# Optimization experiments

Hardware: AMD Instinct MI355X
Metric: run time of the kernel (lower is better)

The kernel has to match this reference:

```python
import jax, jax.numpy as jnp
import numpy as np

N_NODES = 20000
N_EDGES = 320000
IN_DIM = 512
NUM_CLASSES = 10
DROP_P = 0.2


def _gcn_conv(x, src, dst, W, b, n):
    # PyG GCNConv: linear transform, add self-loops, symmetric deg^-1/2 norm,
    # scatter-add into destination nodes, then bias.
    h = x @ W                                   # [N, out]
    loops = jnp.arange(n)
    s = jnp.concatenate([src, loops])           # source (j)
    d = jnp.concatenate([dst, loops])           # destination (i)
    deg = jax.ops.segment_sum(jnp.ones_like(s, dtype=h.dtype), d, num_segments=n)
    dinv = jax.lax.rsqrt(deg)                   # deg >= 1 thanks to self-loops
    norm = dinv[s] * dinv[d]                    # [E+N]
    msg = h[s] * norm[:, None]                  # gather + per-edge scale
    out = jax.ops.segment_sum(msg, d, num_segments=n)  # scatter-add
    return out + b


def _dropout(x, key, p=DROP_P):
    keep = jax.random.bernoulli(key, 1.0 - p, x.shape)
    return jnp.where(keep, x / (1.0 - p), jnp.zeros((), x.dtype))


def setup_inputs() -> dict:
    key = jax.random.key(0)
    ks = jax.random.split(key, 6)
    x = jax.random.normal(ks[0], (N_NODES, IN_DIM), dtype=jnp.float32)
    edge_index = jax.random.randint(ks[1], (2, N_EDGES), 0, N_NODES, dtype=jnp.int64)
    h1, h2 = IN_DIM // 2, IN_DIM // 4
    W1 = jax.random.normal(ks[2], (IN_DIM, h1), dtype=jnp.float32) / np.sqrt(IN_DIM)
    W2 = jax.random.normal(ks[3], (h1, h2), dtype=jnp.float32) / np.sqrt(h1)
    W3 = jax.random.normal(ks[4], (h2, NUM_CLASSES), dtype=jnp.float32) / np.sqrt(h2)
    b1 = jnp.zeros((h1,), jnp.float32)
    b2 = jnp.zeros((h2,), jnp.float32)
    b3 = jnp.zeros((NUM_CLASSES,), jnp.float32)
    return {"x": x, "edge_index": edge_index, "W1": W1, "b1": b1,
            "W2": W2, "b2": b2, "W3": W3, "b3": b3}


def reference(x, edge_index, W1, b1, W2, b2, W3, b3):
    n = x.shape[0]
    src, dst = edge_index[0], edge_index[1]
    dk1, dk2 = jax.random.split(jax.random.key(1))
    h = _gcn_conv(x, src, dst, W1, b1, n)
    h = _dropout(jax.nn.relu(h), dk1)
    h = _gcn_conv(h, src, dst, W2, b2, n)
    h = _dropout(jax.nn.relu(h), dk2)
    h = _gcn_conv(h, src, dst, W3, b3, n)
    return jax.nn.log_softmax(h, axis=1)
```

## Files before the change

### kernel.cpp

```cpp
#include <hip/hip_runtime.h>
#include <hip/hip_bf16.h>
#include <math.h>

typedef __attribute__((ext_vector_type(8))) short short8;
typedef __attribute__((ext_vector_type(8))) unsigned short ushort8;
typedef __attribute__((ext_vector_type(4))) unsigned short ushort4v;
typedef __attribute__((ext_vector_type(2))) unsigned short ushort2v;
typedef __attribute__((ext_vector_type(4))) float f32x4;

__host__ __device__ inline void threefry2x32(unsigned k0, unsigned k1,
                                             unsigned x0, unsigned x1,
                                             unsigned* out0, unsigned* out1) {
  unsigned ks0 = k0, ks1 = k1, ks2 = k0 ^ k1 ^ 0x1BD11BDAu;
  x0 += ks0; x1 += ks1;
#define TF_ROUND(r) { x0 += x1; x1 = (x1 << (r)) | (x1 >> (32 - (r))); x1 ^= x0; }
  TF_ROUND(13) TF_ROUND(15) TF_ROUND(26) TF_ROUND(6)
  x0 += ks1; x1 += ks2 + 1u;
  TF_ROUND(17) TF_ROUND(29) TF_ROUND(16) TF_ROUND(24)
  x0 += ks2; x1 += ks0 + 2u;
  TF_ROUND(13) TF_ROUND(15) TF_ROUND(26) TF_ROUND(6)
  x0 += ks0; x1 += ks1 + 3u;
  TF_ROUND(17) TF_ROUND(29) TF_ROUND(16) TF_ROUND(24)
  x0 += ks1; x1 += ks2 + 4u;
  TF_ROUND(13) TF_ROUND(15) TF_ROUND(26) TF_ROUND(6)
  x0 += ks2; x1 += ks0 + 5u;
#undef TF_ROUND
  *out0 = x0; *out1 = x1;
}

__device__ inline float jax_uniform01(unsigned key0, unsigned key1, unsigned i) {
  unsigned o0, o1;
  threefry2x32(key0, key1, 0u, i, &o0, &o1);
  unsigned bits = o0 ^ o1;
  return __uint_as_float((bits >> 9) | 0x3f800000u) - 1.0f;
}

__device__ inline unsigned short f2bf(float f) {
  unsigned u = __float_as_uint(f);
  u += 0x7fffu + ((u >> 16) & 1u);
  return (unsigned short)(u >> 16);
}

__device__ inline float bf2f(unsigned short b) {
  return __uint_as_float(((unsigned)b) << 16);
}

__global__ void k_zero(int* p, int n) {
  int i = blockIdx.x * blockDim.x + threadIdx.x;
  if (i < n) p[i] = 0;
}

__global__ void k_deg(const int* __restrict__ ei, int E, int* __restrict__ deg) {
  int e = blockIdx.x * blockDim.x + threadIdx.x;
  if (e >= E) return;
  atomicAdd(&deg[ei[E + e]], 1);
}

__global__ void k_scan(const int* __restrict__ deg, int* __restrict__ off, int n) {
  __shared__ int sums[1024];
  int t = threadIdx.x;
  int per = (n + 1023) >> 10;
  int base = t * per;
  int s = 0;
  for (int j = 0; j < per; ++j) { int idx = base + j; if (idx < n) s += deg[idx]; }
  sums[t] = s;
  __syncthreads();
  for (int d = 1; d < 1024; d <<= 1) {
    int v = (t >= d) ? sums[t - d] : 0;
    __syncthreads();
    sums[t] += v;
    __syncthreads();
  }
  int prefix = (t == 0) ? 0 : sums[t - 1];
  for (int j = 0; j < per; ++j) {
    int idx = base + j;
    if (idx < n) { off[idx] = prefix; prefix += deg[idx]; }
  }
  if (t == 1023) off[n] = sums[1023];
}

__global__ void k_prep(const int* __restrict__ deg, const int* __restrict__ off,
                       int* __restrict__ cur, float* __restrict__ dinv, int n) {
  int i = blockIdx.x * blockDim.x + threadIdx.x;
  if (i >= n) return;
  cur[i] = off[i];
  dinv[i] = 1.0f / sqrtf((float)(deg[i] + 1));
}

__global__ void k_fill(const int* __restrict__ ei, int E,
                       int* __restrict__ cur, int* __restrict__ srcs) {
  int e = blockIdx.x * blockDim.x + threadIdx.x;
  if (e >= E) return;
  int s = ei[e];
  int d = ei[E + e];
  int pos = atomicAdd(&cur[d], 1);
  srcs[pos] = s;
}

__global__ void k_cvt_wT(const float* __restrict__ W, unsigned short* __restrict__ WT,
                         int K, int N) {
  int idx = blockIdx.x * blockDim.x + threadIdx.x;
  if (idx >= K * N) return;
  int k = idx / N, n = idx % N;
  WT[(size_t)n * K + k] = f2bf(W[idx]);
}

template <bool AF32, bool OBF>
__global__ __launch_bounds__(256) void k_gemm_mfma(const void* __restrict__ Ap,
                                                   const unsigned short* __restrict__ BT,
                                                   void* __restrict__ Cp,
                                                   int M, int N, int K) {
  __shared__ unsigned short As[64][40];
  __shared__ unsigned short Bs[128][40];
  const int tid = threadIdx.x;
  const int row0 = blockIdx.y * 64;
  const int col0 = blockIdx.x * 128;
  const int w = tid >> 6, lane = tid & 63;
  const int wm = w >> 1, wn = w & 1;
  const int lr = lane & 15, lk = lane >> 4;

  f32x4 acc[2][4];
#pragma unroll
  for (int mi = 0; mi < 2; ++mi)
#pragma unroll
    for (int ni = 0; ni < 4; ++ni) acc[mi][ni] = (f32x4)0.0f;

  const int ar = tid >> 2;
  const int aseg = (tid & 3) * 8;

  for (int k0 = 0; k0 < K; k0 += 32) {
    {
      int grow = row0 + ar;
      ushort8 av = (ushort8)0;
      if (grow < M) {
        if (AF32) {
          const float* A = (const float*)Ap;
          const float* p = &A[(size_t)grow * K + k0 + aseg];
          float4 v0 = *(const float4*)p;
          float4 v1 = *(const float4*)(p + 4);
          av[0] = f2bf(v0.x); av[1] = f2bf(v0.y); av[2] = f2bf(v0.z); av[3] = f2bf(v0.w);
          av[4] = f2bf(v1.x); av[5] = f2bf(v1.y); av[6] = f2bf(v1.z); av[7] = f2bf(v1.w);
        } else {
          const unsigned short* A = (const unsigned short*)Ap;
          av = *(const ushort8*)&A[(size_t)grow * K + k0 + aseg];
        }
      }
      *(ushort8*)&As[ar][aseg] = av;
    }
#pragma unroll
    for (int p = 0; p < 2; ++p) {
      int u = tid + p * 256;
      int br = u >> 2;
      int bseg = (u & 3) * 8;
      ushort8 bv = *(const ushort8*)&BT[(size_t)(col0 + br) * K + k0 + bseg];
      *(ushort8*)&Bs[br][bseg] = bv;
    }
    __syncthreads();

    short8 a[2], b[4];
#pragma unroll
    for (int mi = 0; mi < 2; ++mi)
      a[mi] = *(const short8*)&As[wm * 32 + mi * 16 + lr][lk * 8];
#pragma unroll
    for (int ni = 0; ni < 4; ++ni)
      b[ni] = *(const short8*)&Bs[wn * 64 + ni * 16 + lr][lk * 8];
#pragma unroll
    for (int mi = 0; mi < 2; ++mi)
#pragma unroll
      for (int ni = 0; ni < 4; ++ni)
        acc[mi][ni] = __builtin_amdgcn_mfma_f32_16x16x32_bf16(a[mi], b[ni], acc[mi][ni], 0, 0, 0);
    __syncthreads();
  }

#pragma unroll
  for (int mi = 0; mi < 2; ++mi) {
    int rbase = row0 + wm * 32 + mi * 16 + lk * 4;
#pragma unroll
    for (int j = 0; j < 4; ++j) {
      int row = rbase + j;
      if (row < M) {
#pragma unroll
        for (int ni = 0; ni < 4; ++ni) {
          int col = col0 + wn * 64 + ni * 16 + lr;
          if (OBF) {
            ((unsigned short*)Cp)[(size_t)row * N + col] = f2bf(acc[mi][ni][j]);
          } else {
            ((float*)Cp)[(size_t)row * N + col] = acc[mi][ni][j];
          }
        }
      }
    }
  }
}

__global__ __launch_bounds__(256) void k_gemm(const float* __restrict__ A,
                                              const float* __restrict__ B,
                                              float* __restrict__ C,
                                              int M, int N, int K) {
  __shared__ float As[64][17];
  __shared__ float Bs[16][64];
  const int tid = threadIdx.x;
  const int tx = tid & 15, ty = tid >> 4;
  const int row0 = blockIdx.y * 64, col0 = blockIdx.x * 64;
  const int am = tid >> 2;
  const int aq = (tid & 3) * 4;
  const int bk = tid >> 4;
  const int bg = (tid & 15) * 4;
  const bool nvec = ((N & 3) == 0);
  float acc[4][4] = {{0.f}};

  for (int k0 = 0; k0 < K; k0 += 16) {
    {
      int row = row0 + am;
      if (row < M) {
        const float4 v = *reinterpret_cast<const float4*>(&A[(size_t)row * K + k0 + aq]);
        As[am][aq + 0] = v.x; As[am][aq + 1] = v.y;
        As[am][aq + 2] = v.z; As[am][aq + 3] = v.w;
      } else {
        As[am][aq + 0] = 0.f; As[am][aq + 1] = 0.f;
        As[am][aq + 2] = 0.f; As[am][aq + 3] = 0.f;
      }
    }
    {
      int krow = k0 + bk;
      if (nvec && (col0 + bg + 4 <= N)) {
        const float4 v = *reinterpret_cast<const float4*>(&B[(size_t)krow * N + col0 + bg]);
        Bs[bk][bg + 0] = v.x; Bs[bk][bg + 1] = v.y;
        Bs[bk][bg + 2] = v.z; Bs[bk][bg + 3] = v.w;
      } else {
        for (int j = 0; j < 4; ++j) {
          int col = col0 + bg + j;
          Bs[bk][bg + j] = (col < N) ? B[(size_t)krow * N + col] : 0.f;
        }
      }
    }
    __syncthreads();
#pragma unroll
    for (int kk = 0; kk < 16; ++kk) {
      float a0 = As[ty * 4 + 0][kk];
      float a1 = As[ty * 4 + 1][kk];
      float a2 = As[ty * 4 + 2][kk];
      float a3 = As[ty * 4 + 3][kk];
      float4 bv = *reinterpret_cast<const float4*>(&Bs[kk][tx * 4]);
      acc[0][0] += a0 * bv.x; acc[0][1] += a0 * bv.y; acc[0][2] += a0 * bv.z; acc[0][3] += a0 * bv.w;
      acc[1][0] += a1 * bv.x; acc[1][1] += a1 * bv.y; acc[1][2] += a1 * bv.z; acc[1][3] += a1 * bv.w;
      acc[2][0] += a2 * bv.x; acc[2][1] += a2 * bv.y; acc[2][2] += a2 * bv.z; acc[2][3] += a2 * bv.w;
      acc[3][0] += a3 * bv.x; acc[3][1] += a3 * bv.y; acc[3][2] += a3 * bv.z; acc[3][3] += a3 * bv.w;
    }
    __syncthreads();
  }

  for (int i = 0; i < 4; ++i) {
    int row = row0 + ty * 4 + i;
    if (row >= M) continue;
    for (int j = 0; j < 4; ++j) {
      int col = col0 + tx * 4 + j;
      if (col < N) C[(size_t)row * N + col] = acc[i][j];
    }
  }
}

template <int C, bool OBF>
__global__ __launch_bounds__(256) void k_agg_bf(const unsigned short* __restrict__ h,
                                                void* __restrict__ outv,
                                                const int* __restrict__ off,
                                                const int* __restrict__ srcs,
                                                const float* __restrict__ dinv,
                                                const float* __restrict__ bias,
                                                unsigned key0, unsigned key1, int n) {
  typedef __attribute__((ext_vector_type(C))) unsigned short ushortC;
  const int node = blockIdx.x * (blockDim.x >> 6) + (threadIdx.x >> 6);
  if (node >= n) return;
  const int lane = threadIdx.x & 63;
  const int F = 64 * C;
  const float dv = dinv[node];

  float acc[C];
  {
    ushortC r = *(const ushortC*)(h + (size_t)node * F + lane * C);
    float wv = dv * dv;
#pragma unroll
    for (int j = 0; j < C; ++j) acc[j] = bf2f(r[j]) * wv;
  }
  int e = off[node];
  const int e1 = off[node + 1];
  for (; e + 4 <= e1; e += 4) {
    int s0 = srcs[e + 0], s1 = srcs[e + 1], s2 = srcs[e + 2], s3 = srcs[e + 3];
    float w0 = dinv[s0] * dv, w1 = dinv[s1] * dv, w2 = dinv[s2] * dv, w3 = dinv[s3] * dv;
    ushortC r0 = *(const ushortC*)(h + (size_t)s0 * F + lane * C);
    ushortC r1 = *(const ushortC*)(h + (size_t)s1 * F + lane * C);
    ushortC r2 = *(const ushortC*)(h + (size_t)s2 * F + lane * C);
    ushortC r3 = *(const ushortC*)(h + (size_t)s3 * F + lane * C);
#pragma unroll
    for (int j = 0; j < C; ++j)
      acc[j] += bf2f(r0[j]) * w0 + bf2f(r1[j]) * w1 + bf2f(r2[j]) * w2 + bf2f(r3[j]) * w3;
  }
  for (; e < e1; ++e) {
    int s = srcs[e];
    float wv = dinv[s] * dv;
    ushortC r = *(const ushortC*)(h + (size_t)s * F + lane * C);
#pragma unroll
    for (int j = 0; j < C; ++j) acc[j] += bf2f(r[j]) * wv;
  }
#pragma unroll
  for (int j = 0; j < C; ++j) {
    float v = acc[j] + bias[lane * C + j];
    v = fmaxf(v, 0.0f);
    unsigned i = (unsigned)(node * F + lane * C + j);
    float u = jax_uniform01(key0, key1, i);
    v = (u < 0.8f) ? (v * 1.25f) : 0.0f;
    acc[j] = v;
  }
  if (OBF) {
    unsigned short* op = (unsigned short*)outv + (size_t)node * F + lane * C;
#pragma unroll
    for (int j = 0; j < C; ++j) op[j] = f2bf(acc[j]);
  } else {
    float* op = (float*)outv + (size_t)node * F + lane * C;
#pragma unroll
    for (int j = 0; j < C; ++j) op[j] = acc[j];
  }
}

__global__ void k_agg3_lsm(const float* __restrict__ h, float* __restrict__ out,
                           const int* __restrict__ off, const int* __restrict__ srcs,
                           const float* __restrict__ dinv, const float* __restrict__ b,
                           int n) {
  int d = blockIdx.x * blockDim.x + threadIdx.x;
  if (d >= n) return;
  float acc[10];
  float dv = dinv[d];
#pragma unroll
  for (int f = 0; f < 10; ++f) acc[f] = h[(size_t)d * 10 + f] * dv * dv;
  int e1 = off[d + 1];
  for (int e = off[d]; e < e1; ++e) {
    int s = srcs[e];
    float w = dinv[s] * dv;
#pragma unroll
    for (int f = 0; f < 10; ++f) acc[f] += h[(size_t)s * 10 + f] * w;
  }
  float m = -1e30f;
#pragma unroll
  for (int f = 0; f < 10; ++f) { acc[f] += b[f]; m = fmaxf(m, acc[f]); }
  float sum = 0.f;
#pragma unroll
  for (int f = 0; f < 10; ++f) sum += expf(acc[f] - m);
  float lse = m + logf(sum);
#pragma unroll
  for (int f = 0; f < 10; ++f) out[(size_t)d * 10 + f] = acc[f] - lse;
}

extern "C" void kernel_launch(void* const* d_in, const int* in_sizes, int n_in,
                              void* d_out, int out_size, void* d_ws, size_t ws_size,
                              hipStream_t stream) {
  const float* x  = (const float*)d_in[0];
  const int*   ei = (const int*)d_in[1];
  const float* W1 = (const float*)d_in[2];
  const float* b1 = (const float*)d_in[3];
  const float* W2 = (const float*)d_in[4];
  const float* b2 = (const float*)d_in[5];
  const float* W3 = (const float*)d_in[6];
  const float* b3 = (const float*)d_in[7];
  float* out = (float*)d_out;

  const int N = 20000;
  const int E = in_sizes[1] / 2;
  const int D1 = 256, D2 = 128;

  char* ws = (char*)d_ws;
  auto carve = [&](size_t bytes) -> char* {
    char* p = ws;
    ws += (bytes + 255) & ~(size_t)255;
    return p;
  };
  int*   deg  = (int*)carve((size_t)N * 4);
  int*   off  = (int*)carve((size_t)(N + 1) * 4);
  int*   cur  = (int*)carve((size_t)N * 4);
  float* dinv = (float*)carve((size_t)N * 4);
  int*   srcs = (int*)carve((size_t)E * 4);
  unsigned short* W1T = (unsigned short*)carve((size_t)D1 * 512 * 2);
  unsigned short* W2T = (unsigned short*)carve((size_t)D2 * D1 * 2);
  unsigned short* bufHb = (unsigned short*)carve((size_t)N * D1 * 2);
  unsigned short* bufA_bf = (unsigned short*)carve((size_t)N * D1 * 2);
  float* bufA2 = (float*)bufA_bf;
  float* bufH3 = (float*)carve((size_t)N * 10 * 4);

  unsigned dk1_0, dk1_1, dk2_0, dk2_1;
  threefry2x32(0u, 1u, 0u, 0u, &dk1_0, &dk1_1);
  threefry2x32(0u, 1u, 0u, 1u, &dk2_0, &dk2_1);

  k_zero<<<(N + 255) / 256, 256, 0, stream>>>(deg, N);
  k_deg<<<(E + 255) / 256, 256, 0, stream>>>(ei, E, deg);
  k_scan<<<1, 1024, 0, stream>>>(deg, off, N);
  k_prep<<<(N + 255) / 256, 256, 0, stream>>>(deg, off, cur, dinv, N);
  k_fill<<<(E + 255) / 256, 256, 0, stream>>>(ei, E, cur, srcs);
  k_cvt_wT<<<(512 * D1 + 255) / 256, 256, 0, stream>>>(W1, W1T, 512, D1);
  k_cvt_wT<<<(D1 * D2 + 255) / 256, 256, 0, stream>>>(W2, W2T, D1, D2);

  k_gemm_mfma<true, true><<<dim3(D1 / 128, (N + 63) / 64), 256, 0, stream>>>(x, W1T, bufHb, N, D1, 512);
  k_agg_bf<4, true><<<(N + 3) / 4, 256, 0, stream>>>(bufHb, bufA_bf, off, srcs, dinv, b1, dk1_0, dk1_1, N);

  k_gemm_mfma<false, true><<<dim3(D2 / 128, (N + 63) / 64), 256, 0, stream>>>(bufA_bf, W2T, bufHb, N, D2, D1);
  k_agg_bf<2, false><<<(N + 3) / 4, 256, 0, stream>>>(bufHb, bufA2, off, srcs, dinv, b2, dk2_0, dk2_1, N);

  k_gemm<<<dim3(1, (N + 63) / 64), 256, 0, stream>>>(bufA2, W3, bufH3, N, 10, D2);
  k_agg3_lsm<<<(N + 127) / 128, 128, 0, stream>>>(bufH3, out, off, srcs, dinv, b3, N);
}
```

Baseline: 185.0 us.

## Fuse prep kernels, widen layer-1 GEMM tile, parallelize final aggregation per wavefront

Folds the offset/dinv prep into the single-block scan and merges the two weight conversions into one launch, cutting launch count. The first-layer MFMA GEMM now uses a 256-wide N tile, so each block reads its A rows and converts them from fp32 once instead of twice. The final 10-class aggregation plus log-softmax moves from one thread per node to one wavefront per node with lanes over features, using shuffle reductions. The risks are a longer serial loop in the one-block scan, higher register use in the wider GEMM, and 54 of the 64 lanes idle in the last aggregation.

```diff
diff --git a/kernel.cpp b/kernel.cpp
--- a/kernel.cpp
+++ b/kernel.cpp
@@ -4,8 +4,6 @@
 
 typedef __attribute__((ext_vector_type(8))) short short8;
 typedef __attribute__((ext_vector_type(8))) unsigned short ushort8;
-typedef __attribute__((ext_vector_type(4))) unsigned short ushort4v;
-typedef __attribute__((ext_vector_type(2))) unsigned short ushort2v;
 typedef __attribute__((ext_vector_type(4))) float f32x4;
 
 __host__ __device__ inline void threefry2x32(unsigned k0, unsigned k1,
@@ -56,7 +54,8 @@
   atomicAdd(&deg[ei[E + e]], 1);
 }
 
-__global__ void k_scan(const int* __restrict__ deg, int* __restrict__ off, int n) {
+__global__ void k_scan_prep(const int* __restrict__ deg, int* __restrict__ off,
+                            int* __restrict__ cur, float* __restrict__ dinv, int n) {
   __shared__ int sums[1024];
   int t = threadIdx.x;
   int per = (n + 1023) >> 10;
@@ -74,17 +73,14 @@
   int prefix = (t == 0) ? 0 : sums[t - 1];
   for (int j = 0; j < per; ++j) {
     int idx = base + j;
-    if (idx < n) { off[idx] = prefix; prefix += deg[idx]; }
+    if (idx < n) {
+      off[idx] = prefix;
+      cur[idx] = prefix;
+      dinv[idx] = 1.0f / sqrtf((float)(deg[idx] + 1));
+      prefix += deg[idx];
+    }
   }
   if (t == 1023) off[n] = sums[1023];
-}
-
-__global__ void k_prep(const int* __restrict__ deg, const int* __restrict__ off,
-                       int* __restrict__ cur, float* __restrict__ dinv, int n) {
-  int i = blockIdx.x * blockDim.x + threadIdx.x;
-  if (i >= n) return;
-  cur[i] = off[i];
-  dinv[i] = 1.0f / sqrtf((float)(deg[i] + 1));
 }
 
 __global__ void k_fill(const int* __restrict__ ei, int E,
@@ -97,33 +93,40 @@
   srcs[pos] = s;
 }
 
-__global__ void k_cvt_wT(const float* __restrict__ W, unsigned short* __restrict__ WT,
-                         int K, int N) {
+__global__ void k_cvt_all(const float* __restrict__ W1, unsigned short* __restrict__ W1T,
+                          const float* __restrict__ W2, unsigned short* __restrict__ W2T) {
+  const int S1 = 512 * 256, S2 = 256 * 128;
   int idx = blockIdx.x * blockDim.x + threadIdx.x;
-  if (idx >= K * N) return;
-  int k = idx / N, n = idx % N;
-  WT[(size_t)n * K + k] = f2bf(W[idx]);
-}
-
-template <bool AF32, bool OBF>
+  if (idx < S1) {
+    int k = idx / 256, n = idx % 256;
+    W1T[(size_t)n * 512 + k] = f2bf(W1[idx]);
+  } else if (idx < S1 + S2) {
+    int i2 = idx - S1;
+    int k = i2 / 128, n = i2 % 128;
+    W2T[(size_t)n * 256 + k] = f2bf(W2[i2]);
+  }
+}
+
+template <int NF, bool AF32, bool OBF>
 __global__ __launch_bounds__(256) void k_gemm_mfma(const void* __restrict__ Ap,
                                                    const unsigned short* __restrict__ BT,
                                                    void* __restrict__ Cp,
                                                    int M, int N, int K) {
+  constexpr int BN = 32 * NF;
   __shared__ unsigned short As[64][40];
-  __shared__ unsigned short Bs[128][40];
+  __shared__ unsigned short Bs[BN][40];
   const int tid = threadIdx.x;
   const int row0 = blockIdx.y * 64;
-  const int col0 = blockIdx.x * 128;
+  const int col0 = blockIdx.x * BN;
   const int w = tid >> 6, lane = tid & 63;
   const int wm = w >> 1, wn = w & 1;
   const int lr = lane & 15, lk = lane >> 4;
 
-  f32x4 acc[2][4];
+  f32x4 acc[2][NF];
 #pragma unroll
   for (int mi = 0; mi < 2; ++mi)
 #pragma unroll
-    for (int ni = 0; ni < 4; ++ni) acc[mi][ni] = (f32x4)0.0f;
+    for (int ni = 0; ni < NF; ++ni) acc[mi][ni] = (f32x4)0.0f;
 
   const int ar = tid >> 2;
   const int aseg = (tid & 3) * 8;
@@ -148,7 +151,7 @@
       *(ushort8*)&As[ar][aseg] = av;
     }
 #pragma unroll
-    for (int p = 0; p < 2; ++p) {
+    for (int p = 0; p < BN / 64; ++p) {
       int u = tid + p * 256;
       int br = u >> 2;
       int bseg = (u & 3) * 8;
@@ -157,17 +160,17 @@
     }
     __syncthreads();
 
-    short8 a[2], b[4];
+    short8 a[2], b[NF];
 #pragma unroll
     for (int mi = 0; mi < 2; ++mi)
       a[mi] = *(const short8*)&As[wm * 32 + mi * 16 + lr][lk * 8];
 #pragma unroll
-    for (int ni = 0; ni < 4; ++ni)
-      b[ni] = *(const short8*)&Bs[wn * 64 + ni * 16 + lr][lk * 8];
+    for (int ni = 0; ni < NF; ++ni)
+      b[ni] = *(const short8*)&Bs[wn * (BN / 2) + ni * 16 + lr][lk * 8];
 #pragma unroll
     for (int mi = 0; mi < 2; ++mi)
 #pragma unroll
-      for (int ni = 0; ni < 4; ++ni)
+      for (int ni = 0; ni < NF; ++ni)
         acc[mi][ni] = __builtin_amdgcn_mfma_f32_16x16x32_bf16(a[mi], b[ni], acc[mi][ni], 0, 0, 0);
     __syncthreads();
   }
@@ -180,8 +183,8 @@
       int row = rbase + j;
       if (row < M) {
 #pragma unroll
-        for (int ni = 0; ni < 4; ++ni) {
-          int col = col0 + wn * 64 + ni * 16 + lr;
+        for (int ni = 0; ni < NF; ++ni) {
+          int col = col0 + wn * (BN / 2) + ni * 16 + lr;
           if (OBF) {
             ((unsigned short*)Cp)[(size_t)row * N + col] = f2bf(acc[mi][ni][j]);
           } else {
@@ -322,32 +325,46 @@
   }
 }
 
-__global__ void k_agg3_lsm(const float* __restrict__ h, float* __restrict__ out,
-                           const int* __restrict__ off, const int* __restrict__ srcs,
-                           const float* __restrict__ dinv, const float* __restrict__ b,
-                           int n) {
-  int d = blockIdx.x * blockDim.x + threadIdx.x;
-  if (d >= n) return;
-  float acc[10];
-  float dv = dinv[d];
-#pragma unroll
-  for (int f = 0; f < 10; ++f) acc[f] = h[(size_t)d * 10 + f] * dv * dv;
-  int e1 = off[d + 1];
-  for (int e = off[d]; e < e1; ++e) {
+__global__ __launch_bounds__(256) void k_agg3_lsm_v2(const float* __restrict__ h,
+                                                     float* __restrict__ out,
+                                                     const int* __restrict__ off,
+                                                     const int* __restrict__ srcs,
+                                                     const float* __restrict__ dinv,
+                                                     const float* __restrict__ b,
+                                                     int n) {
+  const int node = blockIdx.x * 4 + (threadIdx.x >> 6);
+  if (node >= n) return;
+  const int lane = threadIdx.x & 63;
+  const bool act = (lane < 10);
+  const float dv = dinv[node];
+
+  float acc = 0.0f;
+  if (act) acc = h[(size_t)node * 10 + lane] * dv * dv;
+  int e = off[node];
+  const int e1 = off[node + 1];
+  for (; e + 4 <= e1; e += 4) {
+    int s0 = srcs[e + 0], s1 = srcs[e + 1], s2 = srcs[e + 2], s3 = srcs[e + 3];
+    float w0 = dinv[s0] * dv, w1 = dinv[s1] * dv, w2 = dinv[s2] * dv, w3 = dinv[s3] * dv;
+    if (act) {
+      acc += h[(size_t)s0 * 10 + lane] * w0 + h[(size_t)s1 * 10 + lane] * w1 +
+             h[(size_t)s2 * 10 + lane] * w2 + h[(size_t)s3 * 10 + lane] * w3;
+    }
+  }
+  for (; e < e1; ++e) {
     int s = srcs[e];
     float w = dinv[s] * dv;
-#pragma unroll
-    for (int f = 0; f < 10; ++f) acc[f] += h[(size_t)s * 10 + f] * w;
-  }
-  float m = -1e30f;
-#pragma unroll
-  for (int f = 0; f < 10; ++f) { acc[f] += b[f]; m = fmaxf(m, acc[f]); }
-  float sum = 0.f;
-#pragma unroll
-  for (int f = 0; f < 10; ++f) sum += expf(acc[f] - m);
-  float lse = m + logf(sum);
-#pragma unroll
-  for (int f = 0; f < 10; ++f) out[(size_t)d * 10 + f] = acc[f] - lse;
+    if (act) acc += h[(size_t)s * 10 + lane] * w;
+  }
+  float v = act ? (acc + b[lane]) : -1e30f;
+  float m = v;
+#pragma unroll
+  for (int o = 32; o; o >>= 1) m = fmaxf(m, __shfl_xor(m, o));
+  float p = act ? expf(v - m) : 0.0f;
+  float ssum = p;
+#pragma unroll
+  for (int o = 32; o; o >>= 1) ssum += __shfl_xor(ssum, o);
+  float lse = m + logf(ssum);
+  if (act) out[(size_t)node * 10 + lane] = v - lse;
 }
 
 extern "C" void kernel_launch(void* const* d_in, const int* in_sizes, int n_in,
@@ -391,18 +408,16 @@
 
   k_zero<<<(N + 255) / 256, 256, 0, stream>>>(deg, N);
   k_deg<<<(E + 255) / 256, 256, 0, stream>>>(ei, E, deg);
-  k_scan<<<1, 1024, 0, stream>>>(deg, off, N);
-  k_prep<<<(N + 255) / 256, 256, 0, stream>>>(deg, off, cur, dinv, N);
+  k_scan_prep<<<1, 1024, 0, stream>>>(deg, off, cur, dinv, N);
   k_fill<<<(E + 255) / 256, 256, 0, stream>>>(ei, E, cur, srcs);
-  k_cvt_wT<<<(512 * D1 + 255) / 256, 256, 0, stream>>>(W1, W1T, 512, D1);
-  k_cvt_wT<<<(D1 * D2 + 255) / 256, 256, 0, stream>>>(W2, W2T, D1, D2);
-
-  k_gemm_mfma<true, true><<<dim3(D1 / 128, (N + 63) / 64), 256, 0, stream>>>(x, W1T, bufHb, N, D1, 512);
+  k_cvt_all<<<(512 * 256 + 256 * 128 + 255) / 256, 256, 0, stream>>>(W1, W1T, W2, W2T);
+
+  k_gemm_mfma<8, true, true><<<dim3(1, (N + 63) / 64), 256, 0, stream>>>(x, W1T, bufHb, N, D1, 512);
   k_agg_bf<4, true><<<(N + 3) / 4, 256, 0, stream>>>(bufHb, bufA_bf, off, srcs, dinv, b1, dk1_0, dk1_1, N);
 
-  k_gemm_mfma<false, true><<<dim3(D2 / 128, (N + 63) / 64), 256, 0, stream>>>(bufA_bf, W2T, bufHb, N, D2, D1);
+  k_gemm_mfma<4, false, true><<<dim3(1, (N + 63) / 64), 256, 0, stream>>>(bufA_bf, W2T, bufHb, N, D2, D1);
   k_agg_bf<2, false><<<(N + 3) / 4, 256, 0, stream>>>(bufHb, bufA2, off, srcs, dinv, b2, dk2_0, dk2_1, N);
 
   k_gemm<<<dim3(1, (N + 63) / 64), 256, 0, stream>>>(bufA2, W3, bufH3, N, 10, D2);
-  k_agg3_lsm<<<(N + 127) / 128, 128, 0, stream>>>(bufH3, out, off, srcs, dinv, b3, N);
-}
+  k_agg3_lsm_v2<<<(N + 3) / 4, 256, 0, stream>>>(bufH3, out, off, srcs, dinv, b3, N);
+}
```

New measurement: 204.3 us. 1.1x slower.
